# Kernel tuning notes

Hardware: AMD Instinct MI355X
Metric: run time of the kernel (lower is better)

The kernel has to match this reference:

```python
import jax, jax.numpy as jnp
import numpy as np

N_NODES = 100000
N_EDGES = 1600000
N_DATE = 5000  # last N_DATE nodes are date nodes [0,0,1]
D_IN = 128
D_H = 128
N_CLASSES = 16
MLP_HID = 8


def setup_inputs() -> dict:
    key = jax.random.key(0)
    ks = jax.random.split(key, 12)
    feature = jax.random.normal(ks[0], (N_NODES, D_IN), dtype=jnp.float32)
    edge_weight = jax.random.uniform(ks[1], (N_EDGES,), dtype=jnp.float32)
    src = jax.random.randint(ks[2], (N_EDGES,), 0, N_NODES, dtype=jnp.int32)
    dst = jax.random.randint(ks[3], (N_EDGES,), 0, N_NODES, dtype=jnp.int32)
    # node_type one-hot: regular nodes [1,0,0], last N_DATE nodes are date nodes [0,0,1]
    nt = np.zeros((N_NODES, 3), dtype=np.int32)
    nt[: N_NODES - N_DATE, 0] = 1
    nt[N_NODES - N_DATE :, 2] = 1
    node_type = jnp.asarray(nt)
    # GraphConv weights (xavier uniform) + zero bias, DGL convention: h @ W, W:[in,out]
    def xavier(k, fan_in, fan_out):
        lim = float(np.sqrt(6.0 / (fan_in + fan_out)))
        return jax.random.uniform(k, (fan_in, fan_out), jnp.float32, -lim, lim)
    W0 = xavier(ks[4], D_IN, D_H)
    b0 = jnp.zeros((D_H,), jnp.float32)
    W1 = xavier(ks[5], D_H, D_H)
    b1 = jnp.zeros((D_H,), jnp.float32)
    mlp_w1 = xavier(ks[6], D_H, MLP_HID)
    mlp_b1 = jnp.zeros((MLP_HID,), jnp.float32)
    mlp_w2 = xavier(ks[7], MLP_HID, N_CLASSES)
    mlp_b2 = jnp.zeros((N_CLASSES,), jnp.float32)
    return {
        "feature": feature, "edge_weight": edge_weight, "src": src, "dst": dst,
        "node_type": node_type, "W0": W0, "b0": b0, "W1": W1, "b1": b1,
        "mlp_w1": mlp_w1, "mlp_b1": mlp_b1, "mlp_w2": mlp_w2, "mlp_b2": mlp_b2,
    }


def reference(feature, edge_weight, src, dst, node_type,
              W0, b0, W1, b1, mlp_w1, mlp_b1, mlp_w2, mlp_b2):
    n = feature.shape[0]
    ones_e = jnp.ones_like(edge_weight)
    # unweighted degrees (DGL norm='both'), clamped to >= 1
    deg_out = jnp.clip(jax.ops.segment_sum(ones_e, src, num_segments=n), 1.0)
    deg_in = jnp.clip(jax.ops.segment_sum(ones_e, dst, num_segments=n), 1.0)
    norm_src = deg_out ** -0.5  # [N]
    norm_dst = deg_in ** -0.5   # [N]

    def graph_conv(h, W, b):
        hn = h * norm_src[:, None]                      # D_out^{-1/2} src scaling
        msg = hn[src] * edge_weight[:, None]            # [E, d] edge-weighted gather
        agg = jax.ops.segment_sum(msg, dst, num_segments=n)  # scatter-add
        return (agg * norm_dst[:, None]) @ W + b        # D_in^{-1/2}, then linear

    h = jax.nn.relu(graph_conv(feature, W0, b0))
    h = jax.nn.relu(graph_conv(h, W1, b1))

    # sum-pool over date nodes ([0,0,1]) == tail slice in original layout
    date_mask = ((node_type[:, 0] == 0) & (node_type[:, 1] == 0) & (node_type[:, 2] == 1)).astype(h.dtype)
    cnt = date_mask.sum()
    pooled = (h * date_mask[:, None]).sum(axis=0) / cnt  # [d_h]

    hid = jax.nn.relu(pooled @ mlp_w1 + mlp_b1)
    return hid @ mlp_w2 + mlp_b2  # [num_classes]
```

## Files before the change

### kernel.cpp

```cpp
#include <hip/hip_runtime.h>
#include <hip/hip_fp16.h>
#include <hip/hip_fp8.h>
#include <stdint.h>

#define D 128
#define GT 16
#define SLOTS 48
#define EPB 4096
#define PTB 1024
#define CAPE 5120
#define MAXB 400
#define MAXDATE 8192
#define WPN 16384

typedef _Float16 f16x8 __attribute__((ext_vector_type(8)));
typedef float    f32x4 __attribute__((ext_vector_type(4)));
typedef float    f32x2 __attribute__((ext_vector_type(2)));

__global__ __launch_bounds__(PTB) void partition_kernel(
    const int* __restrict__ src, const int* __restrict__ dst, const float* __restrict__ ew,
    int* __restrict__ cursorA, int* __restrict__ cursorB,
    int2* __restrict__ ebuf, int* __restrict__ sbuf, int E, int nbk) {
    __shared__ int histA[MAXB], histB[MAXB], baseA[MAXB], baseB[MAXB];
    int tid = threadIdx.x;
    for (int i = tid; i < nbk; i += PTB) { histA[i] = 0; histB[i] = 0; }
    __syncthreads();
    int e0 = blockIdx.x * EPB;
    int dcache[EPB / PTB], scache[EPB / PTB];
    float wcache[EPB / PTB];
    #pragma unroll
    for (int i = 0; i < EPB / PTB; ++i) {
        int e = e0 + i * PTB + tid;
        bool ok = e < E;
        dcache[i] = ok ? dst[e] : -1;
        scache[i] = ok ? src[e] : 0;
        wcache[i] = ok ? ew[e] : 0.f;
        if (ok) {
            atomicAdd(&histA[dcache[i] >> 8], 1);
            atomicAdd(&histB[scache[i] >> 8], 1);
        }
    }
    __syncthreads();
    for (int i = tid; i < nbk; i += PTB) {
        baseA[i] = atomicAdd(&cursorA[i], histA[i]);
        baseB[i] = atomicAdd(&cursorB[i], histB[i]);
        histA[i] = 0; histB[i] = 0;
    }
    __syncthreads();
    #pragma unroll
    for (int i = 0; i < EPB / PTB; ++i) {
        if (dcache[i] >= 0) {
            int d = dcache[i], s = scache[i];
            int bA = d >> 8;
            int pA = baseA[bA] + atomicAdd(&histA[bA], 1);
            if (pA < CAPE) ebuf[(size_t)bA * CAPE + pA] =
                make_int2(s | ((d & 255) << 17), __float_as_int(wcache[i]));
            int bB = s >> 8;
            int pB = baseB[bB] + atomicAdd(&histB[bB], 1);
            if (pB < CAPE) sbuf[(size_t)bB * CAPE + pB] = s;
        }
    }
}

__global__ __launch_bounds__(256) void build_count_kernel(
    const int2* __restrict__ ebuf, const int* __restrict__ cursorA,
    const int* __restrict__ sbuf, const int* __restrict__ cursorB,
    int2* __restrict__ ell, int* __restrict__ deg_in, int* __restrict__ deg_out,
    int n, int nbk) {
    __shared__ int lcur[256];
    int tid = threadIdx.x;
    lcur[tid] = 0;
    __syncthreads();
    if (blockIdx.x < (unsigned)nbk) {
        int b = blockIdx.x;
        int cntE = min(cursorA[b], CAPE);
        const int2* buf = ebuf + (size_t)b * CAPE;
        for (int i = tid; i < cntE; i += 256) {
            int2 r = buf[i];
            int s = r.x & 0x1FFFF;
            int dlow = (r.x >> 17) & 255;
            int slot = atomicAdd(&lcur[dlow], 1);
            int node = (b << 8) + dlow;
            if (slot < SLOTS) ell[(size_t)node * SLOTS + slot] = make_int2(s, r.y);
        }
        __syncthreads();
        int v = (b << 8) + tid;
        if (v < n) deg_in[v] = lcur[tid];
    } else {
        int b = blockIdx.x - nbk;
        int cntS = min(cursorB[b], CAPE);
        const int* buf = sbuf + (size_t)b * CAPE;
        for (int i = tid; i < cntS; i += 256) {
            atomicAdd(&lcur[buf[i] & 255], 1);
        }
        __syncthreads();
        int v = (b << 8) + tid;
        if (v < n) deg_out[v] = lcur[tid];
    }
}

__global__ void norm_flag_kernel(const int* __restrict__ deg_out, const int* __restrict__ deg_in,
                                 const int* __restrict__ node_type,
                                 float* __restrict__ norm_src, float* __restrict__ norm_dst,
                                 int* __restrict__ list, int* __restrict__ cnt,
                                 unsigned char* __restrict__ flag, int n) {
    int v = blockIdx.x * blockDim.x + threadIdx.x;
    if (v < n) {
        float d_o = (float)max(deg_out[v], 1);
        float d_i = (float)max(deg_in[v], 1);
        norm_src[v] = 1.0f / sqrtf(d_o);
        norm_dst[v] = 1.0f / sqrtf(d_i);
        flag[v] = 0;
        int t0 = node_type[v * 3 + 0];
        int t1 = node_type[v * 3 + 1];
        int t2 = node_type[v * 3 + 2];
        if (t0 == 0 && t1 == 0 && t2 == 1) {
            int idx = atomicAdd(cnt, 1);
            list[idx] = v;
        }
    }
}

__global__ __launch_bounds__(256) void mark_kernel(
    const int* __restrict__ list, const int* __restrict__ cnt,
    const int2* __restrict__ ell, const int* __restrict__ deg_in,
    unsigned char* __restrict__ flag) {
    int wave = (blockIdx.x * 256 + threadIdx.x) >> 6;
    int lane = threadIdx.x & 63;
    if (wave >= min(*cnt, MAXDATE)) return;
    int v = __builtin_amdgcn_readfirstlane(list[wave]);
    int m = min(deg_in[v], SLOTS);
    if (lane < m) {
        int s = ell[(size_t)v * SLOTS + lane].x;
        flag[s] = 1;
    }
}

__global__ __launch_bounds__(256) void wpack_kernel(const float* __restrict__ W,
                                                    _Float16* __restrict__ wp,
                                                    int* __restrict__ cursorAB,
                                                    float* __restrict__ pooled,
                                                    int* __restrict__ cnt) {
    int tid = threadIdx.x;
    if (blockIdx.x == 0) {
        for (int i = tid; i < 2 * MAXB; i += 256) cursorAB[i] = 0;
        if (tid < D) pooled[tid] = 0.f;
        if (tid == 0) *cnt = 0;
    }
    int base = blockIdx.x * 256 + tid;
    for (int idx = base; idx < WPN; idx += gridDim.x * 256) {
        int j = idx & 7;
        int l = (idx >> 3) & 63;
        int c = (idx >> 9) & 7;
        int k0b = idx >> 12;
        int q = l >> 4, r = l & 15;
        float w = W[(k0b * 32 + q * 8 + j) * 128 + c * 16 + r];
        _Float16 hi = (_Float16)w;
        wp[idx] = hi;
        wp[idx + WPN] = (_Float16)(w - (float)hi);
    }
}

__global__ __launch_bounds__(256) void gemm_mfma_kernel(
    const float* __restrict__ X, const float* __restrict__ ns,
    const _Float16* __restrict__ wp, unsigned char* __restrict__ P8, int n) {
    int lane = threadIdx.x & 63;
    int wib  = threadIdx.x >> 6;
    int q = lane >> 4, r = lane & 15;
    int row0 = blockIdx.x * 128 + wib * 32;
    if (row0 >= n) return;
    int ra = min(row0 + r,      n - 1);
    int rb = min(row0 + 16 + r, n - 1);
    float sa = ns[ra];
    float sb = ns[rb];

    f32x4 acc[2][8];
    #pragma unroll
    for (int t = 0; t < 2; ++t)
        #pragma unroll
        for (int c = 0; c < 8; ++c)
            acc[t][c] = (f32x4){0.f, 0.f, 0.f, 0.f};

    for (int k0 = 0; k0 < 128; k0 += 32) {
        float4 xa0 = *(const float4*)&X[(size_t)ra * 128 + k0 + q * 8];
        float4 xa1 = *(const float4*)&X[(size_t)ra * 128 + k0 + q * 8 + 4];
        float4 xb0 = *(const float4*)&X[(size_t)rb * 128 + k0 + q * 8];
        float4 xb1 = *(const float4*)&X[(size_t)rb * 128 + k0 + q * 8 + 4];
        f16x8 a0, a1;
        a0[0] = (_Float16)(xa0.x * sa); a0[1] = (_Float16)(xa0.y * sa);
        a0[2] = (_Float16)(xa0.z * sa); a0[3] = (_Float16)(xa0.w * sa);
        a0[4] = (_Float16)(xa1.x * sa); a0[5] = (_Float16)(xa1.y * sa);
        a0[6] = (_Float16)(xa1.z * sa); a0[7] = (_Float16)(xa1.w * sa);
        a1[0] = (_Float16)(xb0.x * sb); a1[1] = (_Float16)(xb0.y * sb);
        a1[2] = (_Float16)(xb0.z * sb); a1[3] = (_Float16)(xb0.w * sb);
        a1[4] = (_Float16)(xb1.x * sb); a1[5] = (_Float16)(xb1.y * sb);
        a1[6] = (_Float16)(xb1.z * sb); a1[7] = (_Float16)(xb1.w * sb);
        const _Float16* wb = wp + (size_t)(k0 >> 5) * 4096 + lane * 8;
        #pragma unroll
        for (int c = 0; c < 8; ++c) {
            f16x8 bh = *(const f16x8*)&wb[c * 512];
            f16x8 bl = *(const f16x8*)&wb[c * 512 + WPN];
            acc[0][c] = __builtin_amdgcn_mfma_f32_16x16x32_f16(a0, bh, acc[0][c], 0, 0, 0);
            acc[0][c] = __builtin_amdgcn_mfma_f32_16x16x32_f16(a0, bl, acc[0][c], 0, 0, 0);
            acc[1][c] = __builtin_amdgcn_mfma_f32_16x16x32_f16(a1, bh, acc[1][c], 0, 0, 0);
            acc[1][c] = __builtin_amdgcn_mfma_f32_16x16x32_f16(a1, bl, acc[1][c], 0, 0, 0);
        }
    }

    #pragma unroll
    for (int t = 0; t < 2; ++t) {
        #pragma unroll
        for (int j = 0; j < 4; ++j) {
            int row = row0 + t * 16 + q * 4 + j;
            if (row < n) {
                #pragma unroll
                for (int c = 0; c < 8; ++c) {
                    __hip_fp8_e4m3 qv((float)acc[t][c][j]);
                    P8[(size_t)row * 128 + c * 16 + r] = qv.__x;
                }
            }
        }
    }
}

__global__ __launch_bounds__(256) void gather1_kernel(
    const unsigned char* __restrict__ P8, const int* __restrict__ deg_in,
    const int2* __restrict__ ell, const float* __restrict__ norm_src,
    const float* __restrict__ norm_dst, const float* __restrict__ bias,
    const unsigned char* __restrict__ flag, __half* __restrict__ h1, int n) {
    int wave = (blockIdx.x * 256 + threadIdx.x) >> 6;
    int lane = threadIdx.x & 63;
    if (wave >= n) return;
    int v = __builtin_amdgcn_readfirstlane(wave);
    int half = lane >> 5;
    int l32  = lane & 31;
    const int2* row = ell + (size_t)v * SLOTS;
    unsigned char fv = flag[v];
    int dg = deg_in[v];
    int4 q[16];
    #pragma unroll
    for (int i = 0; i < 16; ++i) q[i] = *(const int4*)&row[2 * i];
    if (fv == 0) return;
    int m = min(dg, SLOTS);
    const unsigned int* P32 = (const unsigned int*)P8;
    unsigned int r[16];
    float w[16];
    #pragma unroll
    for (int i = 0; i < 16; ++i) {
        bool ok = (2 * i + half) < m;
        int s = ok ? (half ? q[i].z : q[i].x) : 0;
        w[i] = ok ? __int_as_float(half ? q[i].w : q[i].y) : 0.f;
        r[i] = P32[(size_t)s * 32 + l32];
    }
    float4 acc = make_float4(0.f, 0.f, 0.f, 0.f);
    #pragma unroll
    for (int i = 0; i < 16; ++i) {
        f32x2 c0 = __builtin_amdgcn_cvt_pk_f32_fp8((int)r[i], false);
        f32x2 c1 = __builtin_amdgcn_cvt_pk_f32_fp8((int)r[i], true);
        acc.x = fmaf(w[i], c0[0], acc.x);
        acc.y = fmaf(w[i], c0[1], acc.y);
        acc.z = fmaf(w[i], c1[0], acc.z);
        acc.w = fmaf(w[i], c1[1], acc.w);
    }
    if (m > 32) {
        for (int e = 32; e < m; e += 4) {
            int4 qa = *(const int4*)&row[e];
            int4 qb = *(const int4*)&row[e + 2];
            int2 p0 = half ? make_int2(qa.z, qa.w) : make_int2(qa.x, qa.y);
            int2 p1 = half ? make_int2(qb.z, qb.w) : make_int2(qb.x, qb.y);
            bool v0 = (e + half) < m;
            bool v1 = (e + 2 + half) < m;
            int s0 = v0 ? p0.x : 0;
            int s1 = v1 ? p1.x : 0;
            unsigned int r0 = P32[(size_t)s0 * 32 + l32];
            unsigned int r1 = P32[(size_t)s1 * 32 + l32];
            float w0 = v0 ? __int_as_float(p0.y) : 0.f;
            float w1 = v1 ? __int_as_float(p1.y) : 0.f;
            f32x2 c0 = __builtin_amdgcn_cvt_pk_f32_fp8((int)r0, false);
            f32x2 c1 = __builtin_amdgcn_cvt_pk_f32_fp8((int)r0, true);
            f32x2 d0 = __builtin_amdgcn_cvt_pk_f32_fp8((int)r1, false);
            f32x2 d1 = __builtin_amdgcn_cvt_pk_f32_fp8((int)r1, true);
            acc.x = fmaf(w0, c0[0], acc.x); acc.x = fmaf(w1, d0[0], acc.x);
            acc.y = fmaf(w0, c0[1], acc.y); acc.y = fmaf(w1, d0[1], acc.y);
            acc.z = fmaf(w0, c1[0], acc.z); acc.z = fmaf(w1, d1[0], acc.z);
            acc.w = fmaf(w0, c1[1], acc.w); acc.w = fmaf(w1, d1[1], acc.w);
        }
    }
    acc.x += __shfl_xor(acc.x, 32);
    acc.y += __shfl_xor(acc.y, 32);
    acc.z += __shfl_xor(acc.z, 32);
    acc.w += __shfl_xor(acc.w, 32);
    if (half == 0) {
        float nd = norm_dst[v];
        float ns = norm_src[v];
        float4 b4 = ((const float4*)bias)[l32];
        float ra = fmaxf(fmaf(acc.x, nd, b4.x), 0.f) * ns;
        float rb = fmaxf(fmaf(acc.y, nd, b4.y), 0.f) * ns;
        float rc = fmaxf(fmaf(acc.z, nd, b4.z), 0.f) * ns;
        float rd = fmaxf(fmaf(acc.w, nd, b4.w), 0.f) * ns;
        __half2 h0 = __floats2half2_rn(ra, rb);
        __half2 h1v = __floats2half2_rn(rc, rd);
        uint2 u;
        u.x = *(unsigned int*)&h0;
        u.y = *(unsigned int*)&h1v;
        ((uint2*)h1)[(size_t)v * 32 + l32] = u;
    }
}

__global__ __launch_bounds__(256) void gather2_list_kernel(
    const __half* __restrict__ h, const int* __restrict__ deg_in,
    const int2* __restrict__ ell, const float* __restrict__ norm_dst,
    const int* __restrict__ list, const int* __restrict__ cnt,
    float* __restrict__ out) {
    int wave = (blockIdx.x * 256 + threadIdx.x) >> 6;
    int lane = threadIdx.x & 63;
    if (wave >= min(*cnt, MAXDATE)) return;
    int v = __builtin_amdgcn_readfirstlane(list[wave]);
    int half = lane >> 5;
    int l32  = lane & 31;
    const int2* row = ell + (size_t)v * SLOTS;
    int dg = deg_in[v];
    int4 q[16];
    #pragma unroll
    for (int i = 0; i < 16; ++i) q[i] = *(const int4*)&row[2 * i];
    int m = min(dg, SLOTS);
    float2 r[16];
    float w[16];
    #pragma unroll
    for (int i = 0; i < 16; ++i) {
        bool ok = (2 * i + half) < m;
        int s = ok ? (half ? q[i].z : q[i].x) : 0;
        w[i] = ok ? __int_as_float(half ? q[i].w : q[i].y) : 0.f;
        r[i] = ((const float2*)h)[(size_t)s * 32 + l32];
    }
    float4 acc = make_float4(0.f, 0.f, 0.f, 0.f);
    #pragma unroll
    for (int i = 0; i < 16; ++i) {
        float2 a01 = __half22float2(*(const __half2*)&r[i].x);
        float2 a23 = __half22float2(*(const __half2*)&r[i].y);
        acc.x = fmaf(w[i], a01.x, acc.x);
        acc.y = fmaf(w[i], a01.y, acc.y);
        acc.z = fmaf(w[i], a23.x, acc.z);
        acc.w = fmaf(w[i], a23.y, acc.w);
    }
    if (m > 32) {
        for (int e = 32; e < m; e += 4) {
            int4 qa = *(const int4*)&row[e];
            int4 qb = *(const int4*)&row[e + 2];
            int2 p0 = half ? make_int2(qa.z, qa.w) : make_int2(qa.x, qa.y);
            int2 p1 = half ? make_int2(qb.z, qb.w) : make_int2(qb.x, qb.y);
            bool v0 = (e + half) < m;
            bool v1 = (e + 2 + half) < m;
            int s0 = v0 ? p0.x : 0;
            int s1 = v1 ? p1.x : 0;
            float2 raw0 = ((const float2*)h)[(size_t)s0 * 32 + l32];
            float2 raw1 = ((const float2*)h)[(size_t)s1 * 32 + l32];
            float w0 = v0 ? __int_as_float(p0.y) : 0.f;
            float w1 = v1 ? __int_as_float(p1.y) : 0.f;
            float2 a01 = __half22float2(*(const __half2*)&raw0.x);
            float2 a23 = __half22float2(*(const __half2*)&raw0.y);
            float2 b01 = __half22float2(*(const __half2*)&raw1.x);
            float2 b23 = __half22float2(*(const __half2*)&raw1.y);
            acc.x = fmaf(w0, a01.x, acc.x); acc.x = fmaf(w1, b01.x, acc.x);
            acc.y = fmaf(w0, a01.y, acc.y); acc.y = fmaf(w1, b01.y, acc.y);
            acc.z = fmaf(w0, a23.x, acc.z); acc.z = fmaf(w1, b23.x, acc.z);
            acc.w = fmaf(w0, a23.y, acc.w); acc.w = fmaf(w1, b23.y, acc.w);
        }
    }
    acc.x += __shfl_xor(acc.x, 32);
    acc.y += __shfl_xor(acc.y, 32);
    acc.z += __shfl_xor(acc.z, 32);
    acc.w += __shfl_xor(acc.w, 32);
    if (half == 0) {
        float nd = norm_dst[v];
        ((float4*)(out + (size_t)wave * D))[l32] =
            make_float4(acc.x * nd, acc.y * nd, acc.z * nd, acc.w * nd);
    }
}

__global__ __launch_bounds__(256) void gemm_pool_kernel(
    const float* __restrict__ X, const float* __restrict__ W,
    const float* __restrict__ bias, const int* __restrict__ cnt,
    float* __restrict__ pooled) {
    __shared__ float rows[4][GT * D];
    int lane = threadIdx.x & 63;
    int wib  = threadIdx.x >> 6;
    int tile = blockIdx.x * 4 + wib;
    int t0 = tile * GT;
    int m = min(*cnt, MAXDATE);
    if (t0 >= m) return;

    float* rw = rows[wib];
    const float2* X2 = (const float2*)X;
    #pragma unroll
    for (int t = 0; t < GT; ++t) {
        int i = t0 + t;
        float2 r = (i < m) ? X2[(size_t)i * 64 + lane] : make_float2(0.f, 0.f);
        *(float2*)&rw[t * D + 2 * lane] = r;
    }
    __builtin_amdgcn_wave_barrier();

    float2 bb = ((const float2*)bias)[lane];
    float2 acc[GT];
    #pragma unroll
    for (int t = 0; t < GT; ++t) acc[t] = make_float2(0.f, 0.f);

    const float2* W2 = (const float2*)W;
    for (int k = 0; k < D; k += 4) {
        float2 w0 = W2[(k + 0) * 64 + lane];
        float2 w1 = W2[(k + 1) * 64 + lane];
        float2 w2 = W2[(k + 2) * 64 + lane];
        float2 w3 = W2[(k + 3) * 64 + lane];
        #pragma unroll
        for (int t = 0; t < GT; ++t) {
            float4 r = *(const float4*)&rw[t * D + k];
            acc[t].x = fmaf(r.x, w0.x, acc[t].x); acc[t].y = fmaf(r.x, w0.y, acc[t].y);
            acc[t].x = fmaf(r.y, w1.x, acc[t].x); acc[t].y = fmaf(r.y, w1.y, acc[t].y);
            acc[t].x = fmaf(r.z, w2.x, acc[t].x); acc[t].y = fmaf(r.z, w2.y, acc[t].y);
            acc[t].x = fmaf(r.w, w3.x, acc[t].x); acc[t].y = fmaf(r.w, w3.y, acc[t].y);
        }
    }

    float psx = 0.f, psy = 0.f;
    #pragma unroll
    for (int t = 0; t < GT; ++t) {
        if (t0 + t < m) {
            psx += fmaxf(acc[t].x + bb.x, 0.f);
            psy += fmaxf(acc[t].y + bb.y, 0.f);
        }
    }
    atomicAdd(&pooled[2 * lane + 0], psx);
    atomicAdd(&pooled[2 * lane + 1], psy);
}

__global__ void mlp_kernel(const float* __restrict__ pooled, const int* __restrict__ cnt,
                           const float* __restrict__ w1, const float* __restrict__ b1,
                           const float* __restrict__ w2, const float* __restrict__ b2,
                           float* __restrict__ out) {
    __shared__ float hid[8];
    int t = threadIdx.x;
    float inv = 1.0f / (float)(*cnt);
    if (t < 8) {
        float a = b1[t];
        for (int k = 0; k < 128; ++k) a = fmaf(pooled[k] * inv, w1[k * 8 + t], a);
        hid[t] = fmaxf(a, 0.f);
    }
    __syncthreads();
    if (t < 16) {
        float a = b2[t];
        for (int j = 0; j < 8; ++j) a = fmaf(hid[j], w2[j * 16 + t], a);
        out[t] = a;
    }
}

extern "C" void kernel_launch(void* const* d_in, const int* in_sizes, int n_in,
                              void* d_out, int out_size, void* d_ws, size_t ws_size,
                              hipStream_t stream) {
    const float* feature   = (const float*)d_in[0];
    const float* ew        = (const float*)d_in[1];
    const int*   src       = (const int*)d_in[2];
    const int*   dst       = (const int*)d_in[3];
    const int*   node_type = (const int*)d_in[4];
    const float* W0        = (const float*)d_in[5];
    const float* b0        = (const float*)d_in[6];
    const float* W1        = (const float*)d_in[7];
    const float* b1        = (const float*)d_in[8];
    const float* mw1       = (const float*)d_in[9];
    const float* mb1       = (const float*)d_in[10];
    const float* mw2       = (const float*)d_in[11];
    const float* mb2       = (const float*)d_in[12];
    float* out = (float*)d_out;

    const int n = in_sizes[0] / D;
    const int E = in_sizes[1];
    const int NBK = (n + 255) >> 8;

    char* ws = (char*)d_ws;
    size_t off = 0;
    auto alloc = [&](size_t bytes) -> void* {
        void* p = ws + off;
        off = (off + bytes + 255) & ~(size_t)255;
        return p;
    };
    int*           cursorAB = (int*)alloc(2 * MAXB * 4);
    int*           deg_in   = (int*)alloc((size_t)n * 4);
    int*           deg_out  = (int*)alloc((size_t)n * 4);
    float*         norm_src = (float*)alloc((size_t)n * 4);
    float*         norm_dst = (float*)alloc((size_t)n * 4);
    int*           list     = (int*)alloc((size_t)n * 4);
    unsigned char* flag     = (unsigned char*)alloc((size_t)n);
    int2*          ell      = (int2*)alloc(((size_t)n * SLOTS + 8) * 8);
    int2*          ebuf     = (int2*)alloc((size_t)NBK * CAPE * 8);
    int*           sbuf     = (int*)alloc((size_t)NBK * CAPE * 4);
    unsigned char* P8       = (unsigned char*)alloc((size_t)n * D);
    __half*        h1       = (__half*)alloc((size_t)n * D * 2);
    _Float16*      wp       = (_Float16*)alloc(2 * WPN * 2);
    float*         pooled   = (float*)alloc(D * 4);
    int*           cnt      = (int*)alloc(256);
    float*         agg      = (float*)sbuf;

    int* cursorA = cursorAB;
    int* cursorB = cursorAB + MAXB;

    const int TB = 256;
    int pblk = (E + EPB - 1) / EPB;
    int nblk = (n + TB - 1) / TB;

    wpack_kernel<<<16, TB, 0, stream>>>(W0, wp, cursorAB, pooled, cnt);
    partition_kernel<<<pblk, PTB, 0, stream>>>(src, dst, ew, cursorA, cursorB, ebuf, sbuf, E, NBK);
    build_count_kernel<<<2 * NBK, TB, 0, stream>>>(ebuf, cursorA, sbuf, cursorB,
                                                   ell, deg_in, deg_out, n, NBK);
    norm_flag_kernel<<<nblk, TB, 0, stream>>>(deg_out, deg_in, node_type,
                                              norm_src, norm_dst, list, cnt, flag, n);
    mark_kernel<<<(MAXDATE * 64) / TB, TB, 0, stream>>>(list, cnt, ell, deg_in, flag);

    gemm_mfma_kernel<<<(n + 127) / 128, TB, 0, stream>>>(feature, norm_src, wp, P8, n);

    gather1_kernel<<<(n * 64 + TB - 1) / TB, TB, 0, stream>>>(
        P8, deg_in, ell, norm_src, norm_dst, b0, flag, h1, n);

    gather2_list_kernel<<<(MAXDATE * 64) / TB, TB, 0, stream>>>(
        h1, deg_in, ell, norm_dst, list, cnt, agg);
    gemm_pool_kernel<<<((MAXDATE + GT - 1) / GT + 3) / 4, TB, 0, stream>>>(agg, W1, b1, cnt, pooled);

    mlp_kernel<<<1, 64, 0, stream>>>(pooled, cnt, mw1, mb1, mw2, mb2, out);
}
```

Measured before the change: 293.9 us.

## Compact flagged nodes into a list, retile layer-0 GEMM with transposed MFMA

mark_kernel now uses atomicExch on an int flag array, so each newly flagged source node is appended once to a compact list2, with its clamped degree packed into the high bits. gather1 reads only that list instead of launching a wave per node and exiting early on unflagged ones. It also takes a shorter path for nodes with degree at most 16. The layer-0 GEMM uses 16 rows per wave with swapped MFMA operands, so each lane holds 4 consecutive output columns and can write packed fp8 with a single 32-bit store. The costs are atomic contention in mark and more GEMM blocks, while gather1 still launches one wave per node even though most of them now exit immediately.

```diff
diff --git a/kernel.cpp b/kernel.cpp
--- a/kernel.cpp
+++ b/kernel.cpp
@@ -103,7 +103,7 @@
                                  const int* __restrict__ node_type,
                                  float* __restrict__ norm_src, float* __restrict__ norm_dst,
                                  int* __restrict__ list, int* __restrict__ cnt,
-                                 unsigned char* __restrict__ flag, int n) {
+                                 int* __restrict__ flag, int n) {
     int v = blockIdx.x * blockDim.x + threadIdx.x;
     if (v < n) {
         float d_o = (float)max(deg_out[v], 1);
@@ -124,7 +124,7 @@
 __global__ __launch_bounds__(256) void mark_kernel(
     const int* __restrict__ list, const int* __restrict__ cnt,
     const int2* __restrict__ ell, const int* __restrict__ deg_in,
-    unsigned char* __restrict__ flag) {
+    int* __restrict__ flag, int* __restrict__ list2, int* __restrict__ cnt2) {
     int wave = (blockIdx.x * 256 + threadIdx.x) >> 6;
     int lane = threadIdx.x & 63;
     if (wave >= min(*cnt, MAXDATE)) return;
@@ -132,7 +132,12 @@
     int m = min(deg_in[v], SLOTS);
     if (lane < m) {
         int s = ell[(size_t)v * SLOTS + lane].x;
-        flag[s] = 1;
+        int old = atomicExch(&flag[s], 1);
+        if (old == 0) {
+            int ms = min(deg_in[s], SLOTS);
+            int idx = atomicAdd(cnt2, 1);
+            list2[idx] = s | (ms << 17);
+        }
     }
 }
 
@@ -145,7 +150,7 @@
     if (blockIdx.x == 0) {
         for (int i = tid; i < 2 * MAXB; i += 256) cursorAB[i] = 0;
         if (tid < D) pooled[tid] = 0.f;
-        if (tid == 0) *cnt = 0;
+        if (tid == 0) { cnt[0] = 0; cnt[1] = 0; }
     }
     int base = blockIdx.x * 256 + tid;
     for (int idx = base; idx < WPN; idx += gridDim.x * 256) {
@@ -167,132 +172,152 @@
     int lane = threadIdx.x & 63;
     int wib  = threadIdx.x >> 6;
     int q = lane >> 4, r = lane & 15;
-    int row0 = blockIdx.x * 128 + wib * 32;
+    int row0 = blockIdx.x * 64 + wib * 16;
     if (row0 >= n) return;
-    int ra = min(row0 + r,      n - 1);
-    int rb = min(row0 + 16 + r, n - 1);
+    int ra = min(row0 + r, n - 1);
     float sa = ns[ra];
-    float sb = ns[rb];
-
-    f32x4 acc[2][8];
-    #pragma unroll
-    for (int t = 0; t < 2; ++t)
-        #pragma unroll
-        for (int c = 0; c < 8; ++c)
-            acc[t][c] = (f32x4){0.f, 0.f, 0.f, 0.f};
-
-    for (int k0 = 0; k0 < 128; k0 += 32) {
-        float4 xa0 = *(const float4*)&X[(size_t)ra * 128 + k0 + q * 8];
-        float4 xa1 = *(const float4*)&X[(size_t)ra * 128 + k0 + q * 8 + 4];
-        float4 xb0 = *(const float4*)&X[(size_t)rb * 128 + k0 + q * 8];
-        float4 xb1 = *(const float4*)&X[(size_t)rb * 128 + k0 + q * 8 + 4];
-        f16x8 a0, a1;
-        a0[0] = (_Float16)(xa0.x * sa); a0[1] = (_Float16)(xa0.y * sa);
-        a0[2] = (_Float16)(xa0.z * sa); a0[3] = (_Float16)(xa0.w * sa);
-        a0[4] = (_Float16)(xa1.x * sa); a0[5] = (_Float16)(xa1.y * sa);
-        a0[6] = (_Float16)(xa1.z * sa); a0[7] = (_Float16)(xa1.w * sa);
-        a1[0] = (_Float16)(xb0.x * sb); a1[1] = (_Float16)(xb0.y * sb);
-        a1[2] = (_Float16)(xb0.z * sb); a1[3] = (_Float16)(xb0.w * sb);
-        a1[4] = (_Float16)(xb1.x * sb); a1[5] = (_Float16)(xb1.y * sb);
-        a1[6] = (_Float16)(xb1.z * sb); a1[7] = (_Float16)(xb1.w * sb);
-        const _Float16* wb = wp + (size_t)(k0 >> 5) * 4096 + lane * 8;
+
+    float4 x[8];
+    #pragma unroll
+    for (int kb = 0; kb < 4; ++kb) {
+        x[2 * kb]     = *(const float4*)&X[(size_t)ra * 128 + kb * 32 + q * 8];
+        x[2 * kb + 1] = *(const float4*)&X[(size_t)ra * 128 + kb * 32 + q * 8 + 4];
+    }
+    f16x8 a[4];
+    #pragma unroll
+    for (int kb = 0; kb < 4; ++kb) {
+        a[kb][0] = (_Float16)(x[2 * kb].x * sa);
+        a[kb][1] = (_Float16)(x[2 * kb].y * sa);
+        a[kb][2] = (_Float16)(x[2 * kb].z * sa);
+        a[kb][3] = (_Float16)(x[2 * kb].w * sa);
+        a[kb][4] = (_Float16)(x[2 * kb + 1].x * sa);
+        a[kb][5] = (_Float16)(x[2 * kb + 1].y * sa);
+        a[kb][6] = (_Float16)(x[2 * kb + 1].z * sa);
+        a[kb][7] = (_Float16)(x[2 * kb + 1].w * sa);
+    }
+
+    f32x4 acc[8];
+    #pragma unroll
+    for (int c = 0; c < 8; ++c) acc[c] = (f32x4){0.f, 0.f, 0.f, 0.f};
+
+    const _Float16* wb = wp + lane * 8;
+    #pragma unroll
+    for (int c = 0; c < 8; ++c) {
+        #pragma unroll
+        for (int kb = 0; kb < 4; ++kb) {
+            f16x8 bh = *(const f16x8*)&wb[kb * 4096 + c * 512];
+            f16x8 bl = *(const f16x8*)&wb[kb * 4096 + c * 512 + WPN];
+            acc[c] = __builtin_amdgcn_mfma_f32_16x16x32_f16(bh, a[kb], acc[c], 0, 0, 0);
+            acc[c] = __builtin_amdgcn_mfma_f32_16x16x32_f16(bl, a[kb], acc[c], 0, 0, 0);
+        }
+    }
+
+    int row = row0 + r;
+    if (row < n) {
         #pragma unroll
         for (int c = 0; c < 8; ++c) {
-            f16x8 bh = *(const f16x8*)&wb[c * 512];
-            f16x8 bl = *(const f16x8*)&wb[c * 512 + WPN];
-            acc[0][c] = __builtin_amdgcn_mfma_f32_16x16x32_f16(a0, bh, acc[0][c], 0, 0, 0);
-            acc[0][c] = __builtin_amdgcn_mfma_f32_16x16x32_f16(a0, bl, acc[0][c], 0, 0, 0);
-            acc[1][c] = __builtin_amdgcn_mfma_f32_16x16x32_f16(a1, bh, acc[1][c], 0, 0, 0);
-            acc[1][c] = __builtin_amdgcn_mfma_f32_16x16x32_f16(a1, bl, acc[1][c], 0, 0, 0);
-        }
-    }
-
-    #pragma unroll
-    for (int t = 0; t < 2; ++t) {
-        #pragma unroll
-        for (int j = 0; j < 4; ++j) {
-            int row = row0 + t * 16 + q * 4 + j;
-            if (row < n) {
-                #pragma unroll
-                for (int c = 0; c < 8; ++c) {
-                    __hip_fp8_e4m3 qv((float)acc[t][c][j]);
-                    P8[(size_t)row * 128 + c * 16 + r] = qv.__x;
-                }
-            }
+            int w0 = __builtin_amdgcn_cvt_pk_fp8_f32(acc[c][0], acc[c][1], 0, false);
+            int w1 = __builtin_amdgcn_cvt_pk_fp8_f32(acc[c][2], acc[c][3], w0, true);
+            *(unsigned int*)&P8[(size_t)row * 128 + c * 16 + q * 4] = (unsigned int)w1;
         }
     }
 }
 
 __global__ __launch_bounds__(256) void gather1_kernel(
-    const unsigned char* __restrict__ P8, const int* __restrict__ deg_in,
-    const int2* __restrict__ ell, const float* __restrict__ norm_src,
-    const float* __restrict__ norm_dst, const float* __restrict__ bias,
-    const unsigned char* __restrict__ flag, __half* __restrict__ h1, int n) {
+    const unsigned char* __restrict__ P8, const int2* __restrict__ ell,
+    const float* __restrict__ norm_src, const float* __restrict__ norm_dst,
+    const float* __restrict__ bias, const int* __restrict__ list2,
+    const int* __restrict__ cnt2, __half* __restrict__ h1) {
     int wave = (blockIdx.x * 256 + threadIdx.x) >> 6;
     int lane = threadIdx.x & 63;
-    if (wave >= n) return;
-    int v = __builtin_amdgcn_readfirstlane(wave);
+    int nn = __builtin_amdgcn_readfirstlane(*cnt2);
+    if (wave >= nn) return;
+    int pk = __builtin_amdgcn_readfirstlane(list2[wave]);
+    int v = pk & 0x1FFFF;
+    int m = pk >> 17;
     int half = lane >> 5;
     int l32  = lane & 31;
     const int2* row = ell + (size_t)v * SLOTS;
-    unsigned char fv = flag[v];
-    int dg = deg_in[v];
-    int4 q[16];
-    #pragma unroll
-    for (int i = 0; i < 16; ++i) q[i] = *(const int4*)&row[2 * i];
-    if (fv == 0) return;
-    int m = min(dg, SLOTS);
     const unsigned int* P32 = (const unsigned int*)P8;
-    unsigned int r[16];
-    float w[16];
-    #pragma unroll
-    for (int i = 0; i < 16; ++i) {
-        bool ok = (2 * i + half) < m;
-        int s = ok ? (half ? q[i].z : q[i].x) : 0;
-        w[i] = ok ? __int_as_float(half ? q[i].w : q[i].y) : 0.f;
-        r[i] = P32[(size_t)s * 32 + l32];
-    }
+    float nd = norm_dst[v];
+    float ns = norm_src[v];
     float4 acc = make_float4(0.f, 0.f, 0.f, 0.f);
-    #pragma unroll
-    for (int i = 0; i < 16; ++i) {
-        f32x2 c0 = __builtin_amdgcn_cvt_pk_f32_fp8((int)r[i], false);
-        f32x2 c1 = __builtin_amdgcn_cvt_pk_f32_fp8((int)r[i], true);
-        acc.x = fmaf(w[i], c0[0], acc.x);
-        acc.y = fmaf(w[i], c0[1], acc.y);
-        acc.z = fmaf(w[i], c1[0], acc.z);
-        acc.w = fmaf(w[i], c1[1], acc.w);
-    }
-    if (m > 32) {
-        for (int e = 32; e < m; e += 4) {
-            int4 qa = *(const int4*)&row[e];
-            int4 qb = *(const int4*)&row[e + 2];
-            int2 p0 = half ? make_int2(qa.z, qa.w) : make_int2(qa.x, qa.y);
-            int2 p1 = half ? make_int2(qb.z, qb.w) : make_int2(qb.x, qb.y);
-            bool v0 = (e + half) < m;
-            bool v1 = (e + 2 + half) < m;
-            int s0 = v0 ? p0.x : 0;
-            int s1 = v1 ? p1.x : 0;
-            unsigned int r0 = P32[(size_t)s0 * 32 + l32];
-            unsigned int r1 = P32[(size_t)s1 * 32 + l32];
-            float w0 = v0 ? __int_as_float(p0.y) : 0.f;
-            float w1 = v1 ? __int_as_float(p1.y) : 0.f;
-            f32x2 c0 = __builtin_amdgcn_cvt_pk_f32_fp8((int)r0, false);
-            f32x2 c1 = __builtin_amdgcn_cvt_pk_f32_fp8((int)r0, true);
-            f32x2 d0 = __builtin_amdgcn_cvt_pk_f32_fp8((int)r1, false);
-            f32x2 d1 = __builtin_amdgcn_cvt_pk_f32_fp8((int)r1, true);
-            acc.x = fmaf(w0, c0[0], acc.x); acc.x = fmaf(w1, d0[0], acc.x);
-            acc.y = fmaf(w0, c0[1], acc.y); acc.y = fmaf(w1, d0[1], acc.y);
-            acc.z = fmaf(w0, c1[0], acc.z); acc.z = fmaf(w1, d1[0], acc.z);
-            acc.w = fmaf(w0, c1[1], acc.w); acc.w = fmaf(w1, d1[1], acc.w);
-        }
-    }
+
+    if (m <= 16) {
+        int4 q[8];
+        #pragma unroll
+        for (int i = 0; i < 8; ++i) q[i] = *(const int4*)&row[2 * i];
+        unsigned int r[8];
+        float w[8];
+        #pragma unroll
+        for (int i = 0; i < 8; ++i) {
+            bool ok = (2 * i + half) < m;
+            int s = ok ? (half ? q[i].z : q[i].x) : 0;
+            w[i] = ok ? __int_as_float(half ? q[i].w : q[i].y) : 0.f;
+            r[i] = P32[(size_t)s * 32 + l32];
+        }
+        #pragma unroll
+        for (int i = 0; i < 8; ++i) {
+            f32x2 c0 = __builtin_amdgcn_cvt_pk_f32_fp8((int)r[i], false);
+            f32x2 c1 = __builtin_amdgcn_cvt_pk_f32_fp8((int)r[i], true);
+            acc.x = fmaf(w[i], c0[0], acc.x);
+            acc.y = fmaf(w[i], c0[1], acc.y);
+            acc.z = fmaf(w[i], c1[0], acc.z);
+            acc.w = fmaf(w[i], c1[1], acc.w);
+        }
+    } else {
+        int4 q[16];
+        #pragma unroll
+        for (int i = 0; i < 16; ++i) q[i] = *(const int4*)&row[2 * i];
+        unsigned int r[16];
+        float w[16];
+        #pragma unroll
+        for (int i = 0; i < 16; ++i) {
+            bool ok = (2 * i + half) < m;
+            int s = ok ? (half ? q[i].z : q[i].x) : 0;
+            w[i] = ok ? __int_as_float(half ? q[i].w : q[i].y) : 0.f;
+            r[i] = P32[(size_t)s * 32 + l32];
+        }
+        #pragma unroll
+        for (int i = 0; i < 16; ++i) {
+            f32x2 c0 = __builtin_amdgcn_cvt_pk_f32_fp8((int)r[i], false);
+            f32x2 c1 = __builtin_amdgcn_cvt_pk_f32_fp8((int)r[i], true);
+            acc.x = fmaf(w[i], c0[0], acc.x);
+            acc.y = fmaf(w[i], c0[1], acc.y);
+            acc.z = fmaf(w[i], c1[0], acc.z);
+            acc.w = fmaf(w[i], c1[1], acc.w);
+        }
+        if (m > 32) {
+            for (int e = 32; e < m; e += 4) {
+                int4 qa = *(const int4*)&row[e];
+                int4 qb = *(const int4*)&row[e + 2];
+                int2 p0 = half ? make_int2(qa.z, qa.w) : make_int2(qa.x, qa.y);
+                int2 p1 = half ? make_int2(qb.z, qb.w) : make_int2(qb.x, qb.y);
+                bool v0 = (e + half) < m;
+                bool v1 = (e + 2 + half) < m;
+                int s0 = v0 ? p0.x : 0;
+                int s1 = v1 ? p1.x : 0;
+                unsigned int r0 = P32[(size_t)s0 * 32 + l32];
+                unsigned int r1 = P32[(size_t)s1 * 32 + l32];
+                float w0 = v0 ? __int_as_float(p0.y) : 0.f;
+                float w1 = v1 ? __int_as_float(p1.y) : 0.f;
+                f32x2 c0 = __builtin_amdgcn_cvt_pk_f32_fp8((int)r0, false);
+                f32x2 c1 = __builtin_amdgcn_cvt_pk_f32_fp8((int)r0, true);
+                f32x2 d0 = __builtin_amdgcn_cvt_pk_f32_fp8((int)r1, false);
+                f32x2 d1 = __builtin_amdgcn_cvt_pk_f32_fp8((int)r1, true);
+                acc.x = fmaf(w0, c0[0], acc.x); acc.x = fmaf(w1, d0[0], acc.x);
+                acc.y = fmaf(w0, c0[1], acc.y); acc.y = fmaf(w1, d0[1], acc.y);
+                acc.z = fmaf(w0, c1[0], acc.z); acc.z = fmaf(w1, d1[0], acc.z);
+                acc.w = fmaf(w0, c1[1], acc.w); acc.w = fmaf(w1, d1[1], acc.w);
+            }
+        }
+    }
+
     acc.x += __shfl_xor(acc.x, 32);
     acc.y += __shfl_xor(acc.y, 32);
     acc.z += __shfl_xor(acc.z, 32);
     acc.w += __shfl_xor(acc.w, 32);
     if (half == 0) {
-        float nd = norm_dst[v];
-        float ns = norm_src[v];
         float4 b4 = ((const float4*)bias)[l32];
         float ra = fmaxf(fmaf(acc.x, nd, b4.x), 0.f) * ns;
         float rb = fmaxf(fmaf(acc.y, nd, b4.y), 0.f) * ns;
@@ -488,7 +513,8 @@
     float*         norm_src = (float*)alloc((size_t)n * 4);
     float*         norm_dst = (float*)alloc((size_t)n * 4);
     int*           list     = (int*)alloc((size_t)n * 4);
-    unsigned char* flag     = (unsigned char*)alloc((size_t)n);
+    int*           list2    = (int*)alloc((size_t)n * 4);
+    int*           flag     = (int*)alloc((size_t)n * 4);
     int2*          ell      = (int2*)alloc(((size_t)n * SLOTS + 8) * 8);
     int2*          ebuf     = (int2*)alloc((size_t)NBK * CAPE * 8);
     int*           sbuf     = (int*)alloc((size_t)NBK * CAPE * 4);
@@ -501,6 +527,7 @@
 
     int* cursorA = cursorAB;
     int* cursorB = cursorAB + MAXB;
+    int* cnt2    = cnt + 1;
 
     const int TB = 256;
     int pblk = (E + EPB - 1) / EPB;
@@ -512,12 +539,13 @@
                                                    ell, deg_in, deg_out, n, NBK);
     norm_flag_kernel<<<nblk, TB, 0, stream>>>(deg_out, deg_in, node_type,
                                               norm_src, norm_dst, list, cnt, flag, n);
-    mark_kernel<<<(MAXDATE * 64) / TB, TB, 0, stream>>>(list, cnt, ell, deg_in, flag);
-
-    gemm_mfma_kernel<<<(n + 127) / 128, TB, 0, stream>>>(feature, norm_src, wp, P8, n);
+    mark_kernel<<<(MAXDATE * 64) / TB, TB, 0, stream>>>(list, cnt, ell, deg_in,
+                                                        flag, list2, cnt2);
+
+    gemm_mfma_kernel<<<(n + 63) / 64, TB, 0, stream>>>(feature, norm_src, wp, P8, n);
 
     gather1_kernel<<<(n * 64 + TB - 1) / TB, TB, 0, stream>>>(
-        P8, deg_in, ell, norm_src, norm_dst, b0, flag, h1, n);
+        P8, ell, norm_src, norm_dst, b0, list2, cnt2, h1);
 
     gather2_list_kernel<<<(MAXDATE * 64) / TB, TB, 0, stream>>>(
         h1, deg_in, ell, norm_dst, list, cnt, agg);
```

Result: slower. 328.4 us (+11.7%).
